# Performance work log

Measured on AMD Instinct MI355X. Metric: run time of the kernel, lower is better.

Reference implementation:

```python
import jax, jax.numpy as jnp
import numpy as np

NUM_HEADS = 16


def setup_inputs() -> dict:
    key = jax.random.key(0)
    ks = jax.random.split(key, 6)
    B, T, C = 2, 1024, 2048
    H, D = NUM_HEADS, C // NUM_HEADS
    Tc = 1024  # cached tokens
    return {
        "x": jax.random.normal(ks[0], (B, T, C), dtype=jnp.float32),
        "cache_k": jax.random.normal(ks[1], (B, H, Tc, D), dtype=jnp.float32),
        "cache_v": jax.random.normal(ks[2], (B, H, Tc, D), dtype=jnp.float32),
        "W_qkv": jax.random.normal(ks[3], (C, 3 * C), dtype=jnp.float32) * (C ** -0.5),
        "W_proj": jax.random.normal(ks[4], (C, C), dtype=jnp.float32) * (C ** -0.5),
        "b_proj": jnp.zeros((C,), dtype=jnp.float32),
        "seq_start": Tc,
    }


def reference(x, cache_k, cache_v, W_qkv, W_proj, b_proj, seq_start):
    B, T, C = x.shape
    H = NUM_HEADS
    D = C // H
    scale = D ** -0.5

    qkv = (x @ W_qkv).reshape(B, T, 3, H, D)
    # (B, H, T, D)
    q = jnp.transpose(qkv[:, :, 0], (0, 2, 1, 3))
    k = jnp.transpose(qkv[:, :, 1], (0, 2, 1, 3))
    v = jnp.transpose(qkv[:, :, 2], (0, 2, 1, 3))

    # append to KV cache along time axis
    k = jnp.concatenate([cache_k, k], axis=2)
    v = jnp.concatenate([cache_v, v], axis=2)
    k_len = k.shape[2]

    # causal mask on absolute positions: query_pos >= key_pos
    query_pos = seq_start + jnp.arange(T)
    key_pos = jnp.arange(k_len)
    causal = query_pos[:, None] >= key_pos[None, :]  # (T, k_len)

    attn = jnp.einsum("bhqd,bhkd->bhqk", q * scale, k)
    attn = jnp.where(causal[None, None], attn, -jnp.inf)
    attn = jax.nn.softmax(attn, axis=-1)

    out = jnp.einsum("bhqk,bhkd->bhqd", attn, v)
    out = jnp.transpose(out, (0, 2, 1, 3)).reshape(B, T, C)
    out = out @ W_proj + b_proj
    return out, k, v
```

## Files before the change

### kernel.cpp

```cpp
#include <hip/hip_runtime.h>
#include <hip/hip_bf16.h>

typedef __attribute__((ext_vector_type(8))) short bf16x8;
typedef __attribute__((ext_vector_type(4))) float f32x4;
typedef __attribute__((ext_vector_type(16))) float f32x16;

#define DI __device__ __forceinline__

static constexpr int Bb  = 2;
static constexpr int Tt  = 1024;
static constexpr int Cc  = 2048;
static constexpr int Hh  = 16;
static constexpr int Dd  = 128;
static constexpr int TC  = 1024;
static constexpr int CTX = 2048;
static constexpr float QSCALE = 0.08838834764831845f;

DI unsigned short f2bf(float f){
  unsigned u = __builtin_bit_cast(unsigned, f);
  u += 0x7FFFu + ((u >> 16) & 1u);
  return (unsigned short)(u >> 16);
}
DI unsigned pk2(float a, float b){
  return (unsigned)f2bf(a) | ((unsigned)f2bf(b) << 16);
}
DI bf16x8 mk4(unsigned a, unsigned b, unsigned c, unsigned d){
  union{ unsigned u[4]; bf16x8 v; } x;
  x.u[0]=a; x.u[1]=b; x.u[2]=c; x.u[3]=d; return x.v;
}
DI f32x16 mfma32(bf16x8 a, bf16x8 b, f32x16 c){
  return __builtin_amdgcn_mfma_f32_32x32x16_bf16(a, b, c, 0, 0, 0);
}
#define MFMA16(a,b,c) __builtin_amdgcn_mfma_f32_16x16x32_bf16(a,b,c,0,0,0)
DI void gld16(const void* g, void* l){
  __builtin_amdgcn_global_load_lds(
      (const __attribute__((address_space(1))) unsigned int*)g,
      (__attribute__((address_space(3))) unsigned int*)l, 16, 0, 0);
}

template<int MODE>
__global__ __launch_bounds__(256) void transpose_k(
    const float* __restrict__ in, unsigned short* __restrict__ out, int R, int C){
  __shared__ unsigned short tile[32][33];
  size_t boff = (size_t)blockIdx.z * R * C;
  in += boff; out += boff;
  int r0 = blockIdx.y * 32, c0 = blockIdx.x * 32;
  int tx = threadIdx.x & 31, ty = threadIdx.x >> 5;
#pragma unroll
  for(int i=0;i<4;i++){
    int r = r0 + ty + i*8;
    tile[ty + i*8][tx] = f2bf(in[(size_t)r * C + c0 + tx]);
  }
  __syncthreads();
#pragma unroll
  for(int i=0;i<4;i++){
    int c = c0 + ty + i*8;
    int k = r0 + tx;
    int kp;
    if constexpr (MODE == 0)
      kp = (k & ~24) | ((((k>>3)&3) ^ ((c>>1)&3)) << 3);
    else
      kp = (k & ~56) | ((((k>>3)&7) ^ (c&7)) << 3);
    out[(size_t)c * R + kp] = tile[tx][ty + i*8];
  }
}

__global__ __launch_bounds__(256) void xconv_k(
    const float4* __restrict__ x4, unsigned short* __restrict__ xbf){
  int idx = blockIdx.x * 256 + threadIdx.x;
  int m = idx >> 9;
  int c4 = (idx & 511) * 4;
  float4 v = x4[idx];
  int cp = ((((c4>>3) ^ (m&7)) << 3)) | (c4 & 7);
  uint2 p; p.x = pk2(v.x, v.y); p.y = pk2(v.z, v.w);
  *(uint2*)(xbf + (size_t)m * Cc + cp) = p;
}

__global__ __launch_bounds__(256) void cache_copy(
    const float4* __restrict__ ck, const float4* __restrict__ cv,
    float4* __restrict__ ok, float4* __restrict__ ov,
    unsigned short* __restrict__ Kws){
  int idx = blockIdx.x * 256 + threadIdx.x;
  const int per = TC * Dd / 4;
  int bh = idx / per, r = idx - bh * per;
  int dst = bh * (CTX * Dd / 4) + r;
  float4 kv = ck[idx];
  ok[dst] = kv;
  ov[dst] = cv[idx];
  int key = r >> 5, dq = (r & 31) * 4;
  int dp = (((dq>>3) ^ (key&7)) << 3) | (dq & 7);
  uint2 p; p.x = pk2(kv.x, kv.y); p.y = pk2(kv.z, kv.w);
  *(uint2*)(Kws + ((size_t)bh * CTX + key) * Dd + dp) = p;
}

__global__ __launch_bounds__(512) void gemm8_k(
    const unsigned short* __restrict__ A, const unsigned short* __restrict__ BT,
    unsigned short* __restrict__ q_ws, float* __restrict__ out_k,
    float* __restrict__ out_v, unsigned short* __restrict__ Kws){
  constexpr int K = 2048;
  __shared__ unsigned short lds[65536];
  int tid = threadIdx.x, lane = tid & 63, w = tid >> 6;
  int lr = lane & 15, lg = lane >> 4;
  int wm = w >> 2, wn = w & 3;
  int bid = blockIdx.x;
  int swz = (bid & 7) * 24 + (bid >> 3);
  int m0 = (swz & 7) * 256;
  int n0 = (swz >> 3) * 256;

  int r8 = lane >> 3, c8 = (lane & 7) * 8;
  const unsigned short* Asrc = A  + (size_t)(m0 + w*16 + r8)*K + c8;
  const unsigned short* Bsrc = BT + (size_t)(n0 + w*16 + r8)*K + c8;
  unsigned short* ldsA = lds;
  unsigned short* ldsB = lds + 32768;

  auto stgA = [&](int b, int h, int kt){
    const unsigned short* s = Asrc + (size_t)(h*128)*K + kt*64;
    unsigned short* d = ldsA + b*16384 + h*8192 + w*1024;
    gld16(s, d);
    gld16(s + (size_t)8*K, d + 512);
  };
  auto stgB = [&](int b, int h, int kt){
    const unsigned short* s = Bsrc + (size_t)(h*128)*K + kt*64;
    unsigned short* d = ldsB + b*16384 + h*8192 + w*1024;
    gld16(s, d);
    gld16(s + (size_t)8*K, d + 512);
  };

  int ua0 = ( lg      ^ (lr & 7)) * 8;
  int ua1 = ((4 + lg) ^ (lr & 7)) * 8;
  const unsigned short* apA = ldsA + (wm*128 + lr)*64;
  const unsigned short* apB = ldsB + (wn*64  + lr)*64;

  f32x4 acc[8][4];
#pragma unroll
  for(int i=0;i<8;i++)
#pragma unroll
    for(int j=0;j<4;j++) acc[i][j] = (f32x4){0.f,0.f,0.f,0.f};
  bf16x8 bfr[4][2];

  stgA(0,0,0); stgA(0,1,0); stgB(0,0,0); stgB(0,1,0); stgB(1,0,1); stgB(1,1,1);
  asm volatile("s_waitcnt vmcnt(4)" ::: "memory");
  __builtin_amdgcn_s_barrier();

#define PHASE(BUF, Q, STAGE, VM)                                           \
  {                                                                        \
    const unsigned short* pa = apA + (BUF)*16384 + (Q)*2048;               \
    bf16x8 a00 = *(const bf16x8*)(pa + ua0);                               \
    bf16x8 a10 = *(const bf16x8*)(pa + 1024 + ua0);                        \
    bf16x8 a01 = *(const bf16x8*)(pa + ua1);                               \
    bf16x8 a11 = *(const bf16x8*)(pa + 1024 + ua1);                        \
    if((Q) == 0){                                                          \
      const unsigned short* pb = apB + (BUF)*16384;                        \
      _Pragma("unroll")                                                    \
      for(int ni=0;ni<4;ni++){                                             \
        bfr[ni][0] = *(const bf16x8*)(pb + ni*1024 + ua0);                 \
        bfr[ni][1] = *(const bf16x8*)(pb + ni*1024 + ua1);                 \
      }                                                                    \
    }                                                                      \
    STAGE;                                                                 \
    __builtin_amdgcn_s_barrier();                                          \
    asm volatile("s_waitcnt lgkmcnt(0)" ::: "memory");                     \
    __builtin_amdgcn_s_setprio(1);                                         \
    _Pragma("unroll")                                                      \
    for(int ni=0;ni<4;ni++){                                               \
      acc[2*(Q)][ni]   = MFMA16(a00, bfr[ni][0], acc[2*(Q)][ni]);          \
      acc[2*(Q)+1][ni] = MFMA16(a10, bfr[ni][0], acc[2*(Q)+1][ni]);        \
    }                                                                      \
    _Pragma("unroll")                                                      \
    for(int ni=0;ni<4;ni++){                                               \
      acc[2*(Q)][ni]   = MFMA16(a01, bfr[ni][1], acc[2*(Q)][ni]);          \
      acc[2*(Q)+1][ni] = MFMA16(a11, bfr[ni][1], acc[2*(Q)+1][ni]);        \
    }                                                                      \
    __builtin_amdgcn_s_setprio(0);                                         \
    VM;                                                                    \
    __builtin_amdgcn_s_barrier();                                          \
  }

#define VMW asm volatile("s_waitcnt vmcnt(4)" ::: "memory")

#pragma unroll 1
  for(int i=0;i<16;i++){
    int t1 = 2*i+1, t2 = (2*i+2)&31, t3 = (2*i+3)&31;
    PHASE(0, 0, stgA(1,0,t1), );
    PHASE(0, 1, stgA(1,1,t1), );
    PHASE(0, 2, stgB(0,0,t2), );
    PHASE(0, 3, stgB(0,1,t2), VMW);
    PHASE(1, 0, stgA(0,0,t2), );
    PHASE(1, 1, stgA(0,1,t2), );
    PHASE(1, 2, stgB(1,0,t3), );
    PHASE(1, 3, stgB(1,1,t3), VMW);
  }
#undef PHASE
#undef VMW
  asm volatile("s_waitcnt vmcnt(0)" ::: "memory");

#pragma unroll
  for(int mi=0;mi<8;mi++){
#pragma unroll
    for(int ni=0;ni<4;ni++){
      int n = n0 + wn*64 + ni*16 + lr;
      int seg = n >> 11;
      int h = (n >> 7) & 15, d = n & 127;
#pragma unroll
      for(int r=0;r<4;r++){
        int mrow = m0 + wm*128 + mi*16 + lg*4 + r;
        float v = acc[mi][ni][r];
        int b = mrow >> 10, t = mrow & 1023;
        if(seg == 0){
          q_ws[((size_t)(b*Hh + h)*Tt + t)*Dd + d] = f2bf(v * QSCALE);
        } else if(seg == 1){
          int key = TC + t;
          size_t base = (size_t)(b*Hh + h)*CTX + key;
          out_k[base*Dd + d] = v;
          int dp = (((d>>3) ^ (key&7)) << 3) | (d & 7);
          Kws[base*Dd + dp] = f2bf(v);
        } else {
          out_v[((size_t)(b*Hh + h)*CTX + TC + t)*Dd + d] = v;
        }
      }
    }
  }
}

__global__ __launch_bounds__(256) void gemmp_k(
    const unsigned short* __restrict__ A, const unsigned short* __restrict__ BT,
    const float* __restrict__ bias, float* __restrict__ outp){
  constexpr int K = 2048;
  __shared__ unsigned short Al[2][128*32];
  __shared__ unsigned short Bl[2][128*32];
  int tid = threadIdx.x, lane = tid & 63, w = tid >> 6;
  int lr = lane & 15, lg = lane >> 4;
  int m0 = blockIdx.x * 128, n0 = blockIdx.y * 128;
  int wr = (w >> 1) * 64, wc = (w & 1) * 64;
  int swz = (lg ^ ((lr >> 1) & 3)) << 3;

  f32x4 acc[4][4];
#pragma unroll
  for(int i=0;i<4;i++)
#pragma unroll
    for(int j=0;j<4;j++) acc[i][j] = (f32x4){0.f,0.f,0.f,0.f};

  auto stage = [&](int buf, int k0){
#pragma unroll
    for(int li=0; li<2; li++){
      int rb = w*32 + li*16;
      gld16(A  + (size_t)(m0 + rb + (lane>>2))*K + k0 + (lane&3)*8, &Al[buf][rb*32]);
      gld16(BT + (size_t)(n0 + rb + (lane>>2))*K + k0 + (lane&3)*8, &Bl[buf][rb*32]);
    }
  };
  stage(0, 0);
  __syncthreads();
  int buf = 0;
  for(int k0 = 0; k0 < K; k0 += 32){
    if(k0 + 32 < K) stage(buf^1, k0 + 32);
    bf16x8 af[4], bfr[4];
#pragma unroll
    for(int mi=0;mi<4;mi++) af[mi]  = *(const bf16x8*)&Al[buf][(wr+mi*16+lr)*32 + swz];
#pragma unroll
    for(int ni=0;ni<4;ni++) bfr[ni] = *(const bf16x8*)&Bl[buf][(wc+ni*16+lr)*32 + swz];
#pragma unroll
    for(int mi=0;mi<4;mi++)
#pragma unroll
      for(int ni=0;ni<4;ni++)
        acc[mi][ni] = MFMA16(af[mi], bfr[ni], acc[mi][ni]);
    __syncthreads();
    buf ^= 1;
  }

#pragma unroll
  for(int mi=0;mi<4;mi++){
#pragma unroll
    for(int ni=0;ni<4;ni++){
      int n = n0 + wc + ni*16 + lr;
#pragma unroll
      for(int r=0;r<4;r++){
        int mrow = m0 + wr + mi*16 + lg*4 + r;
        outp[(size_t)mrow * Cc + n] = acc[mi][ni][r] + bias[n];
      }
    }
  }
}

__global__ __launch_bounds__(256, 2) void attn_k(
    const unsigned short* __restrict__ q_ws,
    const unsigned short* __restrict__ Kws,
    const unsigned short* __restrict__ Vt,
    float* __restrict__ O0, float* __restrict__ O1,
    float* __restrict__ ml){
  __shared__ unsigned short Kl[2][64*128];
  __shared__ unsigned short Vl[2][128*64];
  int tid = threadIdx.x, lane = tid & 63, w = tid >> 6;
  int l31 = lane & 31, hi = lane >> 5, r7 = l31 & 7;
  int qt = blockIdx.x, split = blockIdx.y, bh = blockIdx.z;
  int q0b = qt * 128, qw0 = q0b + w * 32;
  const unsigned short* Kb = Kws + (size_t)bh * CTX * Dd;
  const unsigned short* Vb = Vt  + (size_t)bh * Dd * CTX;

  const unsigned short* qp = q_ws + ((size_t)bh * Tt + qw0 + l31) * Dd + hi * 8;
  bf16x8 qf[8];
#pragma unroll
  for(int ks=0;ks<8;ks++) qf[ks] = *(const bf16x8*)(qp + ks*16);

  f32x16 o[4];
#pragma unroll
  for(int dt=0;dt<4;dt++)
#pragma unroll
    for(int r=0;r<16;r++) o[dt][r] = 0.f;
  float m = -3e38f, l = 0.f;

  int nts = ((TC + q0b + 128) >> 6) >> 1;

  auto stageK = [&](int buf, int j0){
#pragma unroll
    for(int li=0; li<4; li++){
      gld16(Kb + (size_t)(j0 + w*16 + li*4 + (lane>>4))*Dd + (lane&15)*8,
            &Kl[buf][(w*16 + li*4)*128]);
    }
  };
  auto stageV = [&](int buf, int j0){
#pragma unroll
    for(int li=0; li<4; li++){
      gld16(Vb + (size_t)(w*32 + li*8 + (lane>>3))*CTX + j0 + (lane&7)*8,
            &Vl[buf][(w*32 + li*8)*64]);
    }
  };

  stageK(0, split*64); stageV(0, split*64);
  __syncthreads();
  int buf = 0;
#pragma unroll 1
  for(int t = 0; t < nts; t++){
    int j0 = (2*t + split) * 64;
    if(t + 1 < nts){ stageK(buf^1, j0 + 128); stageV(buf^1, j0 + 128); }

    if(j0 <= TC + qw0 + 31){
      f32x16 s0, s1;
#pragma unroll
      for(int r=0;r<16;r++){ s0[r] = 0.f; s1[r] = 0.f; }
#pragma unroll
      for(int ks=0; ks<8; ks++){
        int ub = ((ks*2 + hi) ^ r7) << 3;
        bf16x8 kf0 = *(const bf16x8*)&Kl[buf][l31*128 + ub];
        bf16x8 kf1 = *(const bf16x8*)&Kl[buf][(32+l31)*128 + ub];
        s0 = mfma32(kf0, qf[ks], s0);
        s1 = mfma32(kf1, qf[ks], s1);
      }
      int qabs = TC + qw0 + l31;
      if(j0 + 63 > TC + qw0){
#pragma unroll
        for(int r=0;r<16;r++){
          int kk = (r&3) + 8*(r>>2) + 4*hi;
          if(j0 + kk > qabs)      s0[r] = -1e30f;
          if(j0 + 32 + kk > qabs) s1[r] = -1e30f;
        }
      }
      float tm = fmaxf(s0[0], s1[0]);
#pragma unroll
      for(int r=1;r<16;r++) tm = fmaxf(tm, fmaxf(s0[r], s1[r]));
      tm = fmaxf(tm, __shfl_xor(tm, 32, 64));
      if(!__all(tm - m <= 8.f)){
        float mn = fmaxf(m, tm);
        float alpha = __expf(m - mn);
        m = mn;
        l *= alpha;
        float ar[16];
#pragma unroll
        for(int r=0;r<16;r++){
          int kk = (r&3) + 8*(r>>2) + 4*hi;
          ar[r] = __shfl(alpha, kk, 64);
        }
#pragma unroll
        for(int dt=0;dt<4;dt++)
#pragma unroll
          for(int r=0;r<16;r++) o[dt][r] *= ar[r];
      }
#pragma unroll
      for(int r=0;r<16;r++){ s0[r] = __expf(s0[r] - m); s1[r] = __expf(s1[r] - m); }
      float ts = 0.f;
#pragma unroll
      for(int r=0;r<16;r++) ts += s0[r] + s1[r];
      ts += __shfl_xor(ts, 32, 64);
      l += ts;
#pragma unroll
      for(int ks16=0; ks16<4; ks16++){
        f32x16 p = (ks16 & 2) ? s1 : s0;
        int fb = (ks16 & 1) * 8;
        unsigned e0 = pk2(p[fb+0], p[fb+1]);
        unsigned e1 = pk2(p[fb+2], p[fb+3]);
        unsigned e2 = pk2(p[fb+4], p[fb+5]);
        unsigned e3 = pk2(p[fb+6], p[fb+7]);
        unsigned x0 = __shfl_xor(e0, 32, 64);
        unsigned x1 = __shfl_xor(e1, 32, 64);
        unsigned x2 = __shfl_xor(e2, 32, 64);
        unsigned x3 = __shfl_xor(e3, 32, 64);
        bf16x8 pa = mk4(hi ? x2 : e0, hi ? x3 : e1, hi ? e2 : x0, hi ? e3 : x1);
        int ub = ((ks16*2 + hi) ^ r7) << 3;
#pragma unroll
        for(int dt=0; dt<4; dt++){
          bf16x8 vf = *(const bf16x8*)&Vl[buf][(dt*32 + l31)*64 + ub];
          o[dt] = mfma32(pa, vf, o[dt]);
        }
      }
    }
    __syncthreads();
    buf ^= 1;
  }

  float* Op = split ? O1 : O0;
#pragma unroll
  for(int dt=0; dt<4; dt++){
#pragma unroll
    for(int r=0; r<16; r++){
      int q = qw0 + (r&3) + 8*(r>>2) + 4*hi;
      Op[((size_t)bh*Tt + q)*Dd + dt*32 + l31] = o[dt][r];
    }
  }
  if(lane < 32){
    float* mlp = ml + (((size_t)split*32 + bh)*Tt + qw0 + l31)*2;
    mlp[0] = m; mlp[1] = l;
  }
}

__global__ __launch_bounds__(256) void combine_k(
    const float* __restrict__ O0, const float* __restrict__ O1,
    const float* __restrict__ ml, unsigned short* __restrict__ attn_ws){
  int tid = threadIdx.x;
  int d = tid & 127, rl = tid >> 7;
  int row = blockIdx.x * 2 + rl;
  int bh = row >> 10, t = row & 1023;
  const float* p0 = ml + ((size_t)bh * Tt + t) * 2;
  const float* p1 = ml + (((size_t)32 + bh) * Tt + t) * 2;
  float m0 = p0[0], l0 = p0[1], m1 = p1[0], l1 = p1[1];
  float M = fmaxf(m0, m1);
  float e0 = __expf(m0 - M), e1 = __expf(m1 - M);
  float inv = 1.f / (l0*e0 + l1*e1);
  size_t off = (size_t)row * Dd + d;
  float v = (O0[off]*e0 + O1[off]*e1) * inv;
  int b = bh >> 4, h = bh & 15;
  int mrow = b * Tt + t;
  int c = h * Dd + d;
  int cp = (c & ~24) | ((((c>>3)&3) ^ ((mrow>>1)&3)) << 3);
  attn_ws[(size_t)mrow * Cc + cp] = f2bf(v);
}

extern "C" void kernel_launch(void* const* d_in, const int* in_sizes, int n_in,
                              void* d_out, int out_size, void* d_ws, size_t ws_size,
                              hipStream_t stream){
  const float* x       = (const float*)d_in[0];
  const float* cache_k = (const float*)d_in[1];
  const float* cache_v = (const float*)d_in[2];
  const float* W_qkv   = (const float*)d_in[3];
  const float* W_proj  = (const float*)d_in[4];
  const float* b_proj  = (const float*)d_in[5];

  float* out   = (float*)d_out;
  float* out_k = out   + (size_t)Bb*Tt*Cc;
  float* out_v = out_k + (size_t)Bb*Hh*CTX*Dd;

  if(ws_size < (size_t)67108864) return;
  char* ws = (char*)d_ws;
  unsigned short* WqkvT  = (unsigned short*)(ws);
  unsigned short* WprojT = (unsigned short*)(ws + 25165824);
  unsigned short* q_ws   = (unsigned short*)(ws + 25165824);
  unsigned short* Kws    = (unsigned short*)(ws + 33554432);
  unsigned short* x_bf   = (unsigned short*)(ws + 50331648);
  unsigned short* Vt_ws  = (unsigned short*)(ws + 50331648);
  unsigned short* attn_ws= (unsigned short*)(ws + 50331648);
  float* O0 = out;
  float* O1 = (float*)(ws);
  float* ml = (float*)(ws + 16777216);

  transpose_k<1><<<dim3(192,64,1), 256, 0, stream>>>(W_qkv, WqkvT, 2048, 6144);
  xconv_k<<<dim3(4096), 256, 0, stream>>>((const float4*)x, x_bf);
  cache_copy<<<dim3(4096), 256, 0, stream>>>((const float4*)cache_k, (const float4*)cache_v,
                                             (float4*)out_k, (float4*)out_v, Kws);
  gemm8_k<<<dim3(192), 512, 0, stream>>>(x_bf, WqkvT, q_ws, out_k, out_v, Kws);
  transpose_k<1><<<dim3(4,64,32), 256, 0, stream>>>(out_v, Vt_ws, 2048, 128);
  attn_k<<<dim3(8,2,32), 256, 0, stream>>>(q_ws, Kws, Vt_ws, O0, O1, ml);
  transpose_k<0><<<dim3(64,64,1), 256, 0, stream>>>(W_proj, WprojT, 2048, 2048);
  combine_k<<<dim3(16384), 256, 0, stream>>>(O0, O1, ml, attn_ws);
  gemmp_k<<<dim3(16,16), 256, 0, stream>>>(attn_ws, WprojT, b_proj, out);
}
```

Baseline: 222.1 us.

## Pad GEMM and V-transpose row strides and store second attention split in bf16

Row strides of the bf16 GEMM operands are padded from 2048 to 2112 elements, and the transposed V buffer from 2048 to 2080, to break power-of-two strides. The aim is to avoid channel or bank conflicts when tiles are staged from global memory. The second attention split's partial output is now stored as bf16 instead of fp32, which halves that write and its read in combine, at some precision cost. The workspace layout is repacked so the padded buffers still fit.

```diff
diff --git a/kernel.cpp b/kernel.cpp
--- a/kernel.cpp
+++ b/kernel.cpp
@@ -14,12 +14,17 @@
 static constexpr int Dd  = 128;
 static constexpr int TC  = 1024;
 static constexpr int CTX = 2048;
+static constexpr int LDP = 2112;
+static constexpr int VS  = 2080;
 static constexpr float QSCALE = 0.08838834764831845f;
 
 DI unsigned short f2bf(float f){
   unsigned u = __builtin_bit_cast(unsigned, f);
   u += 0x7FFFu + ((u >> 16) & 1u);
   return (unsigned short)(u >> 16);
+}
+DI float bf2f(unsigned short s){
+  return __builtin_bit_cast(float, (unsigned)s << 16);
 }
 DI unsigned pk2(float a, float b){
   return (unsigned)f2bf(a) | ((unsigned)f2bf(b) << 16);
@@ -40,10 +45,11 @@
 
 template<int MODE>
 __global__ __launch_bounds__(256) void transpose_k(
-    const float* __restrict__ in, unsigned short* __restrict__ out, int R, int C){
+    const float* __restrict__ in, unsigned short* __restrict__ out,
+    int R, int C, int ostride, size_t oplane){
   __shared__ unsigned short tile[32][33];
-  size_t boff = (size_t)blockIdx.z * R * C;
-  in += boff; out += boff;
+  in  += (size_t)blockIdx.z * R * C;
+  out += (size_t)blockIdx.z * oplane;
   int r0 = blockIdx.y * 32, c0 = blockIdx.x * 32;
   int tx = threadIdx.x & 31, ty = threadIdx.x >> 5;
 #pragma unroll
@@ -61,7 +67,7 @@
       kp = (k & ~24) | ((((k>>3)&3) ^ ((c>>1)&3)) << 3);
     else
       kp = (k & ~56) | ((((k>>3)&7) ^ (c&7)) << 3);
-    out[(size_t)c * R + kp] = tile[tx][ty + i*8];
+    out[(size_t)c * ostride + kp] = tile[tx][ty + i*8];
   }
 }
 
@@ -73,7 +79,7 @@
   float4 v = x4[idx];
   int cp = ((((c4>>3) ^ (m&7)) << 3)) | (c4 & 7);
   uint2 p; p.x = pk2(v.x, v.y); p.y = pk2(v.z, v.w);
-  *(uint2*)(xbf + (size_t)m * Cc + cp) = p;
+  *(uint2*)(xbf + (size_t)m * LDP + cp) = p;
 }
 
 __global__ __launch_bounds__(256) void cache_copy(
@@ -97,7 +103,6 @@
     const unsigned short* __restrict__ A, const unsigned short* __restrict__ BT,
     unsigned short* __restrict__ q_ws, float* __restrict__ out_k,
     float* __restrict__ out_v, unsigned short* __restrict__ Kws){
-  constexpr int K = 2048;
   __shared__ unsigned short lds[65536];
   int tid = threadIdx.x, lane = tid & 63, w = tid >> 6;
   int lr = lane & 15, lg = lane >> 4;
@@ -108,22 +113,22 @@
   int n0 = (swz >> 3) * 256;
 
   int r8 = lane >> 3, c8 = (lane & 7) * 8;
-  const unsigned short* Asrc = A  + (size_t)(m0 + w*16 + r8)*K + c8;
-  const unsigned short* Bsrc = BT + (size_t)(n0 + w*16 + r8)*K + c8;
+  const unsigned short* Asrc = A  + (size_t)(m0 + w*16 + r8)*LDP + c8;
+  const unsigned short* Bsrc = BT + (size_t)(n0 + w*16 + r8)*LDP + c8;
   unsigned short* ldsA = lds;
   unsigned short* ldsB = lds + 32768;
 
   auto stgA = [&](int b, int h, int kt){
-    const unsigned short* s = Asrc + (size_t)(h*128)*K + kt*64;
+    const unsigned short* s = Asrc + (size_t)(h*128)*LDP + kt*64;
     unsigned short* d = ldsA + b*16384 + h*8192 + w*1024;
     gld16(s, d);
-    gld16(s + (size_t)8*K, d + 512);
+    gld16(s + (size_t)8*LDP, d + 512);
   };
   auto stgB = [&](int b, int h, int kt){
-    const unsigned short* s = Bsrc + (size_t)(h*128)*K + kt*64;
+    const unsigned short* s = Bsrc + (size_t)(h*128)*LDP + kt*64;
     unsigned short* d = ldsB + b*16384 + h*8192 + w*1024;
     gld16(s, d);
-    gld16(s + (size_t)8*K, d + 512);
+    gld16(s + (size_t)8*LDP, d + 512);
   };
 
   int ua0 = ( lg      ^ (lr & 7)) * 8;
@@ -244,8 +249,8 @@
 #pragma unroll
     for(int li=0; li<2; li++){
       int rb = w*32 + li*16;
-      gld16(A  + (size_t)(m0 + rb + (lane>>2))*K + k0 + (lane&3)*8, &Al[buf][rb*32]);
-      gld16(BT + (size_t)(n0 + rb + (lane>>2))*K + k0 + (lane&3)*8, &Bl[buf][rb*32]);
+      gld16(A  + (size_t)(m0 + rb + (lane>>2))*LDP + k0 + (lane&3)*8, &Al[buf][rb*32]);
+      gld16(BT + (size_t)(n0 + rb + (lane>>2))*LDP + k0 + (lane&3)*8, &Bl[buf][rb*32]);
     }
   };
   stage(0, 0);
@@ -285,7 +290,7 @@
     const unsigned short* __restrict__ q_ws,
     const unsigned short* __restrict__ Kws,
     const unsigned short* __restrict__ Vt,
-    float* __restrict__ O0, float* __restrict__ O1,
+    float* __restrict__ O0, unsigned short* __restrict__ O1b,
     float* __restrict__ ml){
   __shared__ unsigned short Kl[2][64*128];
   __shared__ unsigned short Vl[2][128*64];
@@ -294,7 +299,7 @@
   int qt = blockIdx.x, split = blockIdx.y, bh = blockIdx.z;
   int q0b = qt * 128, qw0 = q0b + w * 32;
   const unsigned short* Kb = Kws + (size_t)bh * CTX * Dd;
-  const unsigned short* Vb = Vt  + (size_t)bh * Dd * CTX;
+  const unsigned short* Vb = Vt  + (size_t)bh * Dd * VS;
 
   const unsigned short* qp = q_ws + ((size_t)bh * Tt + qw0 + l31) * Dd + hi * 8;
   bf16x8 qf[8];
@@ -320,7 +325,7 @@
   auto stageV = [&](int buf, int j0){
 #pragma unroll
     for(int li=0; li<4; li++){
-      gld16(Vb + (size_t)(w*32 + li*8 + (lane>>3))*CTX + j0 + (lane&7)*8,
+      gld16(Vb + (size_t)(w*32 + li*8 + (lane>>3))*VS + j0 + (lane&7)*8,
             &Vl[buf][(w*32 + li*8)*64]);
     }
   };
@@ -406,14 +411,22 @@
     buf ^= 1;
   }
 
-  float* Op = split ? O1 : O0;
-#pragma unroll
-  for(int dt=0; dt<4; dt++){
-#pragma unroll
-    for(int r=0; r<16; r++){
-      int q = qw0 + (r&3) + 8*(r>>2) + 4*hi;
-      Op[((size_t)bh*Tt + q)*Dd + dt*32 + l31] = o[dt][r];
-    }
+  if(split == 0){
+#pragma unroll
+    for(int dt=0; dt<4; dt++)
+#pragma unroll
+      for(int r=0; r<16; r++){
+        int q = qw0 + (r&3) + 8*(r>>2) + 4*hi;
+        O0[((size_t)bh*Tt + q)*Dd + dt*32 + l31] = o[dt][r];
+      }
+  } else {
+#pragma unroll
+    for(int dt=0; dt<4; dt++)
+#pragma unroll
+      for(int r=0; r<16; r++){
+        int q = qw0 + (r&3) + 8*(r>>2) + 4*hi;
+        O1b[((size_t)bh*Tt + q)*Dd + dt*32 + l31] = f2bf(o[dt][r]);
+      }
   }
   if(lane < 32){
     float* mlp = ml + (((size_t)split*32 + bh)*Tt + qw0 + l31)*2;
@@ -422,7 +435,7 @@
 }
 
 __global__ __launch_bounds__(256) void combine_k(
-    const float* __restrict__ O0, const float* __restrict__ O1,
+    const float* __restrict__ O0, const unsigned short* __restrict__ O1b,
     const float* __restrict__ ml, unsigned short* __restrict__ attn_ws){
   int tid = threadIdx.x;
   int d = tid & 127, rl = tid >> 7;
@@ -435,12 +448,12 @@
   float e0 = __expf(m0 - M), e1 = __expf(m1 - M);
   float inv = 1.f / (l0*e0 + l1*e1);
   size_t off = (size_t)row * Dd + d;
-  float v = (O0[off]*e0 + O1[off]*e1) * inv;
+  float v = (O0[off]*e0 + bf2f(O1b[off])*e1) * inv;
   int b = bh >> 4, h = bh & 15;
   int mrow = b * Tt + t;
   int c = h * Dd + d;
   int cp = (c & ~24) | ((((c>>3)&3) ^ ((mrow>>1)&3)) << 3);
-  attn_ws[(size_t)mrow * Cc + cp] = f2bf(v);
+  attn_ws[(size_t)mrow * LDP + cp] = f2bf(v);
 }
 
 extern "C" void kernel_launch(void* const* d_in, const int* in_sizes, int n_in,
@@ -460,24 +473,27 @@
   if(ws_size < (size_t)67108864) return;
   char* ws = (char*)d_ws;
   unsigned short* WqkvT  = (unsigned short*)(ws);
-  unsigned short* WprojT = (unsigned short*)(ws + 25165824);
-  unsigned short* q_ws   = (unsigned short*)(ws + 25165824);
-  unsigned short* Kws    = (unsigned short*)(ws + 33554432);
-  unsigned short* x_bf   = (unsigned short*)(ws + 50331648);
-  unsigned short* Vt_ws  = (unsigned short*)(ws + 50331648);
-  unsigned short* attn_ws= (unsigned short*)(ws + 50331648);
-  float* O0 = out;
-  float* O1 = (float*)(ws);
-  float* ml = (float*)(ws + 16777216);
-
-  transpose_k<1><<<dim3(192,64,1), 256, 0, stream>>>(W_qkv, WqkvT, 2048, 6144);
+  unsigned short* Vt_ws  = (unsigned short*)(ws);
+  unsigned short* attn_ws= (unsigned short*)(ws);
+  unsigned short* WprojT = (unsigned short*)(ws + 17039360);
+  unsigned short* Kws    = (unsigned short*)(ws + 25952256);
+  unsigned short* q_ws   = (unsigned short*)(ws + 42729472);
+  unsigned short* x_bf   = (unsigned short*)(ws + 51118080);
+  unsigned short* O1b    = (unsigned short*)(ws + 51118080);
+  float*          ml     = (float*)(ws + 59768832);
+  float*          O0     = out;
+
+  transpose_k<1><<<dim3(192,64,1), 256, 0, stream>>>(W_qkv, WqkvT, 2048, 6144,
+                                                     LDP, (size_t)6144*LDP);
   xconv_k<<<dim3(4096), 256, 0, stream>>>((const float4*)x, x_bf);
   cache_copy<<<dim3(4096), 256, 0, stream>>>((const float4*)cache_k, (const float4*)cache_v,
                                              (float4*)out_k, (float4*)out_v, Kws);
   gemm8_k<<<dim3(192), 512, 0, stream>>>(x_bf, WqkvT, q_ws, out_k, out_v, Kws);
-  transpose_k<1><<<dim3(4,64,32), 256, 0, stream>>>(out_v, Vt_ws, 2048, 128);
-  attn_k<<<dim3(8,2,32), 256, 0, stream>>>(q_ws, Kws, Vt_ws, O0, O1, ml);
-  transpose_k<0><<<dim3(64,64,1), 256, 0, stream>>>(W_proj, WprojT, 2048, 2048);
-  combine_k<<<dim3(16384), 256, 0, stream>>>(O0, O1, ml, attn_ws);
+  transpose_k<1><<<dim3(4,64,32), 256, 0, stream>>>(out_v, Vt_ws, 2048, 128,
+                                                    VS, (size_t)128*VS);
+  attn_k<<<dim3(8,2,32), 256, 0, stream>>>(q_ws, Kws, Vt_ws, O0, O1b, ml);
+  transpose_k<0><<<dim3(64,64,1), 256, 0, stream>>>(W_proj, WprojT, 2048, 2048,
+                                                    LDP, (size_t)2048*LDP);
+  combine_k<<<dim3(16384), 256, 0, stream>>>(O0, O1b, ml, attn_ws);
   gemmp_k<<<dim3(16,16), 256, 0, stream>>>(attn_ws, WprojT, b_proj, out);
 }
```

Result: no change. 219.6 us (-1.2%).
